# Optimization experiments

Hardware: AMD Instinct MI355X
Metric: run time of the kernel (lower is better)

The kernel has to match this reference:

```python
import jax, jax.numpy as jnp
import numpy as np

N_HEAD = 16
CHUNK = 128  # block size for the causal linear-attention scan


def _phi(x):
    return jax.nn.elu(x) + 1.0


def setup_inputs() -> dict:
    key = jax.random.key(0)
    k1, k2, k3 = jax.random.split(key, 3)
    B, T, E = 4, 2048, 1024
    x = jax.random.normal(k1, (B, T, E), dtype=jnp.float32)
    w_attn = jax.random.normal(k2, (3 * E, E), dtype=jnp.float32) * 0.02
    w_proj = jax.random.normal(k3, (E, E), dtype=jnp.float32) * 0.02
    return {"x": x, "w_attn": w_attn, "w_proj": w_proj}


def _causal_linear_attn(qp, kp, v):
    # qp, kp, v: [B, H, T, D]; phi already applied to qp, kp
    B, H, T, D = qp.shape
    NC = T // CHUNK

    def to_chunks(a):  # -> [NC, B, H, CHUNK, D]
        return a.reshape(B, H, NC, CHUNK, D).transpose(2, 0, 1, 3, 4)

    qc, kc, vc = to_chunks(qp), to_chunks(kp), to_chunks(v)
    mask = jnp.tril(jnp.ones((CHUNK, CHUNK), dtype=bool))

    def step(carry, blk):
        S, z = carry  # S: [B,H,D,D] = sum_{prev} k v^T ; z: [B,H,D] = sum_{prev} k
        q_c, k_c, v_c = blk  # [B,H,CHUNK,D]
        scores = jnp.einsum('bhcd,bhkd->bhck', q_c, k_c)
        scores = jnp.where(mask, scores, 0.0)
        num = (jnp.einsum('bhck,bhke->bhce', scores, v_c)
               + jnp.einsum('bhcd,bhde->bhce', q_c, S))
        den = scores.sum(-1) + jnp.einsum('bhcd,bhd->bhc', q_c, z)
        S = S + jnp.einsum('bhkd,bhke->bhde', k_c, v_c)
        z = z + k_c.sum(axis=2)
        return (S, z), (num, den)

    S0 = jnp.zeros((B, H, D, D), dtype=qp.dtype)
    z0 = jnp.zeros((B, H, D), dtype=qp.dtype)
    _, (num, den) = jax.lax.scan(step, (S0, z0), (qc, kc, vc))
    y = num / (den[..., None] + 1e-6)  # [NC,B,H,CHUNK,D]
    y = y.transpose(1, 2, 0, 3, 4).reshape(B, H, T, D)
    return y


def reference(x, w_attn, w_proj):
    B, T, E = x.shape
    H = N_HEAD
    D = E // H
    qkv = x @ w_attn.T  # [B,T,3E]
    q, k, v = jnp.split(qkv, 3, axis=2)

    def heads(a):  # [B,T,E] -> [B,H,T,D]
        return a.reshape(B, T, H, D).transpose(0, 2, 1, 3)

    y = _causal_linear_attn(_phi(heads(q)), _phi(heads(k)), heads(v))
    y = y.transpose(0, 2, 1, 3).reshape(B, T, E)
    return y @ w_proj.T
```

## Files before the change

### kernel.cpp

```cpp
#include <hip/hip_runtime.h>
#include <math.h>

#define B_ 4
#define T_ 2048
#define E_ 1024
#define H_ 16
#define D_ 64
#define CHUNK_ 128
#define NC_ 16
#define BH_ (B_ * H_)
#define M_ (B_ * T_)

typedef __attribute__((ext_vector_type(8))) short bf16x8;
typedef __attribute__((ext_vector_type(4))) float f32x4;

__device__ __forceinline__ ushort rnbf(float f) {
  unsigned u = __float_as_uint(f);
  unsigned r = (u + 0x7FFFu + ((u >> 16) & 1u)) >> 16;
  return (ushort)r;
}

__device__ __forceinline__ float bf2f(short s) {
  return __uint_as_float(((unsigned)(ushort)s) << 16);
}

__device__ __forceinline__ void gload_lds16(const void* g, void* l) {
  __builtin_amdgcn_global_load_lds(
      (const __attribute__((address_space(1))) unsigned int*)g,
      (__attribute__((address_space(3))) unsigned int*)l, 16, 0, 0);
}

#define VMW(N) do { asm volatile("s_waitcnt vmcnt(" #N ")" ::: "memory"); \
                    __builtin_amdgcn_sched_barrier(0); } while (0)
#define BARR() do { __builtin_amdgcn_s_barrier(); \
                    __builtin_amdgcn_sched_barrier(0); } while (0)
#define LGK0() do { asm volatile("s_waitcnt lgkmcnt(0)" ::: "memory"); \
                    __builtin_amdgcn_sched_barrier(0); } while (0)

#define N4X_ (M_ * E_ / 4)
#define N4A_ (3 * E_ * E_ / 4)
#define N4P_ (E_ * E_ / 4)
__global__ __launch_bounds__(256) void k_cvt3(
    const float* __restrict__ x, const float* __restrict__ wa,
    const float* __restrict__ wp, ushort* __restrict__ xb,
    ushort* __restrict__ wab, ushort* __restrict__ wpb) {
  int i = blockIdx.x * 256 + threadIdx.x;
  const float* src;
  ushort* dst;
  int off;
  if (i < N4X_) { src = x; dst = xb; off = i; }
  else if (i < N4X_ + N4A_) { src = wa; dst = wab; off = i - N4X_; }
  else { src = wp; dst = wpb; off = i - (N4X_ + N4A_); }
  float4 v = ((const float4*)src)[off];
  ushort4 o;
  o.x = rnbf(v.x); o.y = rnbf(v.y); o.z = rnbf(v.z); o.w = rnbf(v.w);
  ((ushort4*)dst)[off] = o;
}

#define ABASE(sl_) ((sl_) * 4096)
#define BBASE(sl_) (8192 + (sl_) * 8192)

#define STG(sl_, tt_) { \
  gload_lds16(Asrc + (tt_) * 32, &lds[ABASE(sl_) + tid * 8]); \
  gload_lds16(Bsrc0 + (tt_) * 32, &lds[BBASE(sl_) + tid * 8]); \
  gload_lds16(Bsrc1 + (tt_) * 32, &lds[BBASE(sl_) + tid * 8 + 4096]); }

#define LDFRAGS(sl_) \
  const ushort* pa = &lds[ABASE(sl_) + aOff]; \
  a0 = *(const bf16x8*)pa;          a1 = *(const bf16x8*)(pa + 512); \
  a2 = *(const bf16x8*)(pa + 1024); a3 = *(const bf16x8*)(pa + 1536); \
  const ushort* pb = &lds[BBASE(sl_) + bOff]; \
  b0 = *(const bf16x8*)pb;          b1 = *(const bf16x8*)(pb + 512); \
  b2 = *(const bf16x8*)(pb + 1024); b3 = *(const bf16x8*)(pb + 1536);

#define MM(i, j, A_, B_) \
  acc[i][j] = __builtin_amdgcn_mfma_f32_16x16x32_bf16(A_, B_, acc[i][j], 0, 0, 0)
#define MFMA16() do { __builtin_amdgcn_s_setprio(1); \
  MM(0,0,a0,b0); MM(0,1,a0,b1); MM(0,2,a0,b2); MM(0,3,a0,b3); \
  MM(1,0,a1,b0); MM(1,1,a1,b1); MM(1,2,a1,b2); MM(1,3,a1,b3); \
  MM(2,0,a2,b0); MM(2,1,a2,b1); MM(2,2,a2,b2); MM(2,3,a2,b3); \
  MM(3,0,a3,b0); MM(3,1,a3,b1); MM(3,2,a3,b2); MM(3,3,a3,b3); \
  __builtin_amdgcn_s_setprio(0); } while (0)

__device__ __forceinline__ void pipe_gemm(const ushort* __restrict__ Ag,
                                          const ushort* __restrict__ Bg,
                                          ushort* lds, f32x4 acc[4][4]) {
  const int tid = threadIdx.x;
  const int l = tid & 63, wv = tid >> 6;
  const int wm = wv >> 2, wn = wv & 3;
  const int c16 = l & 15, g4 = l >> 4;
  const int gch = (tid & 3) ^ ((tid >> 3) & 3);
  const ushort* Asrc = Ag + (size_t)(tid >> 2) * 1024 + gch * 8;
  const ushort* Bsrc0 = Bg + (size_t)(tid >> 2) * 1024 + gch * 8;
  const ushort* Bsrc1 = Bsrc0 + (size_t)128 * 1024;
  const int xq = (c16 >> 1) & 3;
  const int aOff = (wm * 64 + c16) * 32 + ((g4 ^ xq) << 3);
  const int bOff = (wn * 64 + c16) * 32 + ((g4 ^ xq) << 3);

  STG(0, 0);
  STG(1, 1);
#pragma unroll 2
  for (int t = 0; t < 30; ++t) {
    const int sl = t & 1;
    VMW(3); BARR();
    bf16x8 a0, a1, a2, a3, b0, b1, b2, b3;
    LDFRAGS(sl);
    MFMA16();
    BARR();
    STG(sl, t + 2);
  }
  {
    VMW(3); BARR();
    bf16x8 a0, a1, a2, a3, b0, b1, b2, b3;
    LDFRAGS(0);
    MFMA16();
  }
  {
    VMW(0); BARR();
    bf16x8 a0, a1, a2, a3, b0, b1, b2, b3;
    LDFRAGS(1);
    MFMA16();
  }
}

__global__ __launch_bounds__(512, 4) void k_qkv2(
    const ushort* __restrict__ xb, const ushort* __restrict__ wab,
    ushort* __restrict__ qg, ushort* __restrict__ kg,
    ushort* __restrict__ ktg, ushort* __restrict__ vtg,
    float* __restrict__ zp) {
  extern __shared__ ushort lds[];
  const int b = blockIdx.x;
  const int xcd = b & 7, idx = b >> 3;
  const int bm = xcd * 8 + (idx & 7);
  const int bn = idx >> 3;
  const int tid = threadIdx.x;
  const int wv = tid >> 6, l = tid & 63;
  const int wm = wv >> 2, wn = wv & 3;
  const int c16 = l & 15, g4 = l >> 4;

  f32x4 acc[4][4] = {};
  pipe_gemm(xb + (size_t)bm * 128 * 1024, wab + (size_t)bn * 256 * 1024, lds, acc);

  BARR();
  const int colbase = bn * 256 + wn * 64;
  const int which = colbase >> 10;
  const int h = (colbase & 1023) >> 6;
  const int rowbase = bm * 128 + wm * 64;
  const int bidx = rowbase >> 11;
  const int tbase = rowbase & 2047;
  const size_t bh = (size_t)(bidx * 16 + h);
  ushort* wlds2 = &lds[8192 + wv * 2048];
  ushort* tg = (which == 1) ? ktg : vtg;
  float zpart[4] = {0.f, 0.f, 0.f, 0.f};
#pragma unroll
  for (int p = 0; p < 2; ++p) {
#pragma unroll
    for (int mh = 0; mh < 2; ++mh) {
      const int mf = p * 2 + mh;
#pragma unroll
      for (int nf = 0; nf < 4; ++nf) {
        float o[4];
#pragma unroll
        for (int j = 0; j < 4; ++j) {
          float u = acc[mf][nf][j];
          o[j] = (which < 2) ? ((u > 0.f) ? u + 1.f : expf(u)) : u;
        }
        const int d = nf * 16 + c16;
        if (which == 1) zpart[nf] += o[0] + o[1] + o[2] + o[3];
        if (which <= 1) {
          ushort* dst = (which == 0) ? qg : kg;
          const size_t rb = (bh * 2048 + tbase + mf * 16 + g4 * 4) * 64 + d;
#pragma unroll
          for (int j = 0; j < 4; ++j) dst[rb + (size_t)j * 64] = rnbf(o[j]);
        }
        if (which >= 1) {
          const int tb2 = (mh * 4 + g4) ^ (d & 7);
          ushort4 pk;
          pk.x = rnbf(o[0]); pk.y = rnbf(o[1]); pk.z = rnbf(o[2]); pk.w = rnbf(o[3]);
          *(ushort4*)&wlds2[d * 32 + tb2 * 4] = pk;
        }
      }
    }
    if (which >= 1) {
      LGK0();
#pragma unroll
      for (int rt = 0; rt < 4; ++rt) {
        const int d = rt * 16 + (l >> 2);
        const int t0 = (l & 3) * 8;
        const int ba = ((l & 3) * 2) ^ (d & 7);
        const int bb = ((l & 3) * 2 + 1) ^ (d & 7);
        ushort4 ua = *(const ushort4*)&wlds2[d * 32 + ba * 4];
        ushort4 ub = *(const ushort4*)&wlds2[d * 32 + bb * 4];
        __align__(16) ushort tmp[8] = {ua.x, ua.y, ua.z, ua.w,
                                       ub.x, ub.y, ub.z, ub.w};
        *(bf16x8*)&tg[(bh * 64 + d) * 2048 + tbase + p * 32 + t0] =
            *(const bf16x8*)tmp;
      }
      LGK0();
    }
  }
  if (which == 1) {
    const int cc = tbase >> 7;
#pragma unroll
    for (int nf = 0; nf < 4; ++nf) {
      float zz = zpart[nf];
      zz += __shfl_xor(zz, 16);
      zz += __shfl_xor(zz, 32);
      if (l < 16) zp[((bh * NC_ + cc) * 2 + wm) * 64 + nf * 16 + l] = zz;
    }
  }
}

__global__ __launch_bounds__(512, 4) void k_proj2(
    const ushort* __restrict__ yb, const ushort* __restrict__ wpb,
    float* __restrict__ out) {
  extern __shared__ ushort lds[];
  const int b = blockIdx.x;
  const int xcd = b & 7, idx = b >> 3;
  const int bm = xcd * 8 + (idx & 7);
  const int bn = idx >> 3;
  const int tid = threadIdx.x;
  const int wv = tid >> 6, l = tid & 63;
  const int wm = wv >> 2, wn = wv & 3;
  const int c16 = l & 15, g4 = l >> 4;

  f32x4 acc[4][4] = {};
  pipe_gemm(yb + (size_t)bm * 128 * 1024, wpb + (size_t)bn * 256 * 1024, lds, acc);

  const int rowbase = bm * 128 + wm * 64 + g4 * 4;
  const int colbase = bn * 256 + wn * 64 + c16;
#pragma unroll
  for (int mf = 0; mf < 4; ++mf)
#pragma unroll
    for (int nf = 0; nf < 4; ++nf) {
      const size_t base = (size_t)(rowbase + mf * 16) * 1024 + colbase + nf * 16;
#pragma unroll
      for (int j = 0; j < 4; ++j)
        out[base + (size_t)j * 1024] = acc[mf][nf][j];
    }
}

__global__ __launch_bounds__(256) void k_stats(const ushort* __restrict__ ktg,
                                               const ushort* __restrict__ vtg,
                                               float* __restrict__ Sc) {
  __shared__ __align__(16) ushort kT_s[64 * 128], vT_s[64 * 128];
  const int blk = blockIdx.x;
  const int bh = blk >> 4, c = blk & 15;
  const int tid = threadIdx.x;
  const int w = tid >> 6, l = tid & 63;
  const ushort* ktb = ktg + (size_t)bh * D_ * T_ + c * CHUNK_;
  const ushort* vtb = vtg + (size_t)bh * D_ * T_ + c * CHUNK_;
#pragma unroll
  for (int s2 = 0; s2 < 4; ++s2) {
    const int seg = w * 4 + s2;
    const int row = seg * 4 + (l >> 4);
    const int sb = ((l & 15) ^ (row & 7)) * 8;
    gload_lds16(ktb + (size_t)row * T_ + sb, &kT_s[seg * 512]);
    gload_lds16(vtb + (size_t)row * T_ + sb, &vT_s[seg * 512]);
  }
  __syncthreads();
  const int wr = w >> 1, wc = w & 1;
  f32x4 acc[2][2] = {};
#pragma unroll
  for (int kt = 0; kt < 4; ++kt) {
    const int g = kt * 32 + (l >> 4) * 8;
    bf16x8 av[2], bk[2];
#pragma unroll
    for (int rt = 0; rt < 2; ++rt) {
      const int e = wr * 32 + rt * 16 + (l & 15);
      av[rt] = *(const bf16x8*)&vT_s[e * 128 + (g ^ ((e & 7) << 3))];
    }
#pragma unroll
    for (int ct = 0; ct < 2; ++ct) {
      const int d = wc * 32 + ct * 16 + (l & 15);
      bk[ct] = *(const bf16x8*)&kT_s[d * 128 + (g ^ ((d & 7) << 3))];
    }
#pragma unroll
    for (int rt = 0; rt < 2; ++rt)
#pragma unroll
      for (int ct = 0; ct < 2; ++ct)
        acc[rt][ct] = __builtin_amdgcn_mfma_f32_16x16x32_bf16(av[rt], bk[ct],
                                                              acc[rt][ct], 0, 0, 0);
  }
  float* So = Sc + (size_t)blk * 4096;
#pragma unroll
  for (int rt = 0; rt < 2; ++rt)
#pragma unroll
    for (int ct = 0; ct < 2; ++ct)
#pragma unroll
      for (int jj = 0; jj < 4; ++jj)
        So[(wr * 32 + rt * 16 + (l >> 4) * 4 + jj) * 64 + wc * 32 + ct * 16 + (l & 15)] =
            acc[rt][ct][jj];
}

__global__ __launch_bounds__(256) void k_prefix2(const float* __restrict__ Sc,
                                                 ushort* __restrict__ STb,
                                                 const float* __restrict__ zp,
                                                 float* __restrict__ zout) {
  const int b = blockIdx.x;
  const int tid = threadIdx.x;
  if (b < 256) {
    const int bh = b >> 2, qt = b & 3;
    const float4* Sb = (const float4*)(Sc + (size_t)bh * NC_ * 4096) + qt * 256 + tid;
    ushort4* Ob = (ushort4*)(STb + (size_t)bh * NC_ * 4096) + qt * 256 + tid;
    float4 v[16];
#pragma unroll
    for (int c = 0; c < NC_; ++c) v[c] = Sb[c * 1024];
    float4 acc = make_float4(0.f, 0.f, 0.f, 0.f);
#pragma unroll
    for (int c = 0; c < NC_; ++c) {
      ushort4 o;
      o.x = rnbf(acc.x); o.y = rnbf(acc.y); o.z = rnbf(acc.z); o.w = rnbf(acc.w);
      Ob[c * 1024] = o;
      acc.x += v[c].x; acc.y += v[c].y; acc.z += v[c].z; acc.w += v[c].w;
    }
  } else {
    const int bh = b - 256;
    if (tid < 16) {
      const float4* zpb = (const float4*)(zp + (size_t)bh * NC_ * 128);
      float4* zob = (float4*)(zout + (size_t)bh * NC_ * 64);
      float4 t0[16], t1[16];
#pragma unroll
      for (int c = 0; c < NC_; ++c) {
        t0[c] = zpb[c * 32 + tid];
        t1[c] = zpb[c * 32 + 16 + tid];
      }
      float4 za = make_float4(0.f, 0.f, 0.f, 0.f);
#pragma unroll
      for (int c = 0; c < NC_; ++c) {
        zob[c * 16 + tid] = za;
        za.x += t0[c].x + t1[c].x; za.y += t0[c].y + t1[c].y;
        za.z += t0[c].z + t1[c].z; za.w += t0[c].w + t1[c].w;
      }
    }
  }
}

__global__ __launch_bounds__(512, 4) void k_out(
    const ushort* __restrict__ qg, const ushort* __restrict__ kg,
    const ushort* __restrict__ vtg, const ushort* __restrict__ STb,
    const float* __restrict__ zg, ushort* __restrict__ yb) {
  __shared__ __align__(16) ushort k_s[128 * 64];
  __shared__ __align__(16) ushort vT_s[64 * 128];
  __shared__ __align__(16) ushort ST_s[64 * 64];
  __shared__ __align__(16) ushort P_s[128 * 128];
  __shared__ float z_s[64];
  __shared__ float dinter_s[128];
  const int blk = blockIdx.x;
  const int bh = blk >> 4, c = blk & 15;
  const int tid = threadIdx.x;
  const int w = tid >> 6, l = tid & 63;

  const ushort* kbase = kg + ((size_t)bh * T_ + c * CHUNK_) * D_;
  const ushort* vbase = vtg + (size_t)bh * D_ * T_ + c * CHUNK_;
  const ushort* sbase = STb + ((size_t)bh * NC_ + c) * 4096;
  {
    int seg = w, row = seg * 8 + (l >> 3);
    gload_lds16(kbase + (size_t)row * 64 + ((l & 7) ^ (row & 7)) * 8, &k_s[seg * 512]);
    seg = w + 8; row = seg * 8 + (l >> 3);
    gload_lds16(kbase + (size_t)row * 64 + ((l & 7) ^ (row & 7)) * 8, &k_s[seg * 512]);
  }
  {
    int seg = w, row = seg * 4 + (l >> 4);
    gload_lds16(vbase + (size_t)row * T_ + ((l & 15) ^ (row & 7)) * 8, &vT_s[seg * 512]);
    seg = w + 8; row = seg * 4 + (l >> 4);
    gload_lds16(vbase + (size_t)row * T_ + ((l & 15) ^ (row & 7)) * 8, &vT_s[seg * 512]);
  }
  {
    const int seg = w, row = seg * 8 + (l >> 3);
    gload_lds16(sbase + (size_t)row * 64 + ((l & 7) ^ (row & 7)) * 8, &ST_s[seg * 512]);
  }
  if (tid < 64) z_s[tid] = zg[((size_t)bh * NC_ + c) * 64 + tid];
  const int arow = w * 16 + (l & 15);
  const ushort* qrow = qg + ((size_t)bh * T_ + c * CHUNK_ + arow) * D_ + (l >> 4) * 8;
  bf16x8 qf0 = *(const bf16x8*)(qrow);
  bf16x8 qf1 = *(const bf16x8*)(qrow + 32);
  __syncthreads();

  f32x4 sc[8] = {};
#pragma unroll
  for (int jt = 0; jt < 8; ++jt) {
    const int j = jt * 16 + (l & 15);
    const int sw = (j & 7) << 3, g = (l >> 4) * 8;
    bf16x8 b0 = *(const bf16x8*)&k_s[j * 64 + (g ^ sw)];
    bf16x8 b1 = *(const bf16x8*)&k_s[j * 64 + ((g + 32) ^ sw)];
    sc[jt] = __builtin_amdgcn_mfma_f32_16x16x32_bf16(qf0, b0, sc[jt], 0, 0, 0);
    sc[jt] = __builtin_amdgcn_mfma_f32_16x16x32_bf16(qf1, b1, sc[jt], 0, 0, 0);
  }
  const int crow0 = w * 16 + (l >> 4) * 4;
  float rsum[4] = {0.f, 0.f, 0.f, 0.f};
#pragma unroll
  for (int jt = 0; jt < 8; ++jt) {
    const int j = jt * 16 + (l & 15);
#pragma unroll
    for (int jj = 0; jj < 4; ++jj) {
      const int i = crow0 + jj;
      float s = (j <= i) ? sc[jt][jj] : 0.f;
      rsum[jj] += s;
      P_s[i * 128 + (j ^ ((i & 7) << 3))] = rnbf(s);
    }
  }
  float di = 0.f;
#pragma unroll
  for (int jj = 0; jj < 8; ++jj) {
    di = fmaf(bf2f(qf0[jj]), z_s[(l >> 4) * 8 + jj], di);
    di = fmaf(bf2f(qf1[jj]), z_s[32 + (l >> 4) * 8 + jj], di);
  }
  di += __shfl_xor(di, 16);
  di += __shfl_xor(di, 32);
  if (l < 16) dinter_s[w * 16 + l] = di;
#pragma unroll
  for (int jj = 0; jj < 4; ++jj) {
    float r = rsum[jj];
    r += __shfl_xor(r, 1); r += __shfl_xor(r, 2);
    r += __shfl_xor(r, 4); r += __shfl_xor(r, 8);
    rsum[jj] = r;
  }
  __syncthreads();

  f32x4 acc2[4] = {};
#pragma unroll
  for (int et = 0; et < 4; ++et) {
    const int e = et * 16 + (l & 15);
    const int sw = (e & 7) << 3, g = (l >> 4) * 8;
    bf16x8 s0 = *(const bf16x8*)&ST_s[e * 64 + (g ^ sw)];
    bf16x8 s1 = *(const bf16x8*)&ST_s[e * 64 + ((g + 32) ^ sw)];
    acc2[et] = __builtin_amdgcn_mfma_f32_16x16x32_bf16(qf0, s0, acc2[et], 0, 0, 0);
    acc2[et] = __builtin_amdgcn_mfma_f32_16x16x32_bf16(qf1, s1, acc2[et], 0, 0, 0);
  }
  const int prow = w * 16 + (l & 15);
  const int psw = (prow & 7) << 3;
#pragma unroll
  for (int jkt = 0; jkt < 4; ++jkt) {
    bf16x8 pa = *(const bf16x8*)&P_s[prow * 128 + ((jkt * 32 + (l >> 4) * 8) ^ psw)];
#pragma unroll
    for (int et = 0; et < 4; ++et) {
      const int e = et * 16 + (l & 15);
      bf16x8 bv = *(const bf16x8*)&vT_s[e * 128 +
                                        ((jkt * 32 + (l >> 4) * 8) ^ ((e & 7) << 3))];
      acc2[et] = __builtin_amdgcn_mfma_f32_16x16x32_bf16(pa, bv, acc2[et], 0, 0, 0);
    }
  }
  float inv[4];
#pragma unroll
  for (int jj = 0; jj < 4; ++jj)
    inv[jj] = 1.0f / (rsum[jj] + dinter_s[crow0 + jj] + 1e-6f);
  const int b = bh >> 4, h = bh & 15;
#pragma unroll
  for (int et = 0; et < 4; ++et) {
    const int d = et * 16 + (l & 15);
#pragma unroll
    for (int jj = 0; jj < 4; ++jj) {
      const int t = c * CHUNK_ + crow0 + jj;
      yb[((size_t)(b * T_ + t) * H_ + h) * D_ + d] = rnbf(acc2[et][jj] * inv[jj]);
    }
  }
}

extern "C" void kernel_launch(void* const* d_in, const int* in_sizes, int n_in,
                              void* d_out, int out_size, void* d_ws, size_t ws_size,
                              hipStream_t stream) {
  const float* x = (const float*)d_in[0];
  const float* w_attn = (const float*)d_in[1];
  const float* w_proj = (const float*)d_in[2];
  float* out = (float*)d_out;

  ushort* xb = (ushort*)d_ws;
  ushort* wab = xb + (size_t)M_ * E_;
  ushort* wpb = wab + (size_t)3 * E_ * E_;
  ushort* qb = wpb + (size_t)E_ * E_;
  ushort* kbm = qb + (size_t)M_ * E_;
  ushort* kT = kbm + (size_t)M_ * E_;
  ushort* vT = kT + (size_t)M_ * E_;
  ushort* yb = vT + (size_t)M_ * E_;
  ushort* STb = yb + (size_t)M_ * E_;
  float* Schunk = (float*)(STb + (size_t)BH_ * NC_ * 4096);
  float* zpart = Schunk + (size_t)BH_ * NC_ * 4096;
  float* zout = zpart + (size_t)BH_ * NC_ * 2 * 64;

  k_cvt3<<<12288, 256, 0, stream>>>(x, w_attn, w_proj, xb, wab, wpb);

  hipFuncSetAttribute((const void*)k_qkv2,
                      hipFuncAttributeMaxDynamicSharedMemorySize, 49152);
  hipFuncSetAttribute((const void*)k_proj2,
                      hipFuncAttributeMaxDynamicSharedMemorySize, 49152);

  k_qkv2<<<768, 512, 49152, stream>>>(xb, wab, qb, kbm, kT, vT, zpart);
  k_stats<<<1024, 256, 0, stream>>>(kT, vT, Schunk);
  k_prefix2<<<320, 256, 0, stream>>>(Schunk, STb, zpart, zout);
  k_out<<<1024, 512, 0, stream>>>(qb, kbm, vT, STb, zout, yb);
  k_proj2<<<256, 512, 49152, stream>>>(yb, wpb, out);
}
```

Before: 132.4 us.

## Enlarge QKV GEMM tile to 256x256 with deeper K-step and 128KB LDS

Replaces the 128x256-tile QKV projection GEMM with a 256x256 tile that consumes 64-wide K steps per double-buffered stage and uses 128KB of dynamic LDS. Each wave now computes 128x64 outputs, which raises arithmetic intensity and halves global/LDS operand traffic per flop. It also adds setprio around MFMA bursts. Because each wave now covers a whole 128-row chunk, the per-chunk z partial shrinks from two halves to one, and the prefix kernel is simplified to match. The costs are fewer blocks (384, about 1.5 per CU), lower occupancy from launch_bounds(512,2) plus large LDS, and higher register pressure from 32 accumulators.

```diff
diff --git a/kernel.cpp b/kernel.cpp
--- a/kernel.cpp
+++ b/kernel.cpp
@@ -39,7 +39,6 @@
 
 #define N4X_ (M_ * E_ / 4)
 #define N4A_ (3 * E_ * E_ / 4)
-#define N4P_ (E_ * E_ / 4)
 __global__ __launch_bounds__(256) void k_cvt3(
     const float* __restrict__ x, const float* __restrict__ wa,
     const float* __restrict__ wp, ushort* __restrict__ xb,
@@ -57,6 +56,153 @@
   ((ushort4*)dst)[off] = o;
 }
 
+#define STG3(buf_, tt_) { \
+  gload_lds16(Asrc3  + (size_t)(tt_) * 64,          &lds[(buf_) * 32768 + tid * 8]); \
+  gload_lds16(Asrc3  + (size_t)(tt_) * 64 + 131072, &lds[(buf_) * 32768 + 4096 + tid * 8]); \
+  gload_lds16(Asrc3b + (size_t)(tt_) * 64,          &lds[(buf_) * 32768 + 8192 + tid * 8]); \
+  gload_lds16(Asrc3b + (size_t)(tt_) * 64 + 131072, &lds[(buf_) * 32768 + 12288 + tid * 8]); \
+  gload_lds16(Bsrc3  + (size_t)(tt_) * 64,          &lds[(buf_) * 32768 + 16384 + tid * 8]); \
+  gload_lds16(Bsrc3  + (size_t)(tt_) * 64 + 131072, &lds[(buf_) * 32768 + 20480 + tid * 8]); \
+  gload_lds16(Bsrc3b + (size_t)(tt_) * 64,          &lds[(buf_) * 32768 + 24576 + tid * 8]); \
+  gload_lds16(Bsrc3b + (size_t)(tt_) * 64 + 131072, &lds[(buf_) * 32768 + 28672 + tid * 8]); }
+
+#define MM3(i, j, A_, B_) \
+  acc[i][j] = __builtin_amdgcn_mfma_f32_16x16x32_bf16(A_, B_, acc[i][j], 0, 0, 0)
+
+#define CMP_KH(buf_, kh_) do { \
+  const ushort* ap_ = &lds[(buf_) * 32768 + (kh_) * 8192 + aB3]; \
+  const ushort* bp_ = &lds[(buf_) * 32768 + 16384 + (kh_) * 8192 + bB3]; \
+  bf16x8 B0 = *(const bf16x8*)bp_;          bf16x8 B1 = *(const bf16x8*)(bp_ + 512); \
+  bf16x8 B2 = *(const bf16x8*)(bp_ + 1024); bf16x8 B3 = *(const bf16x8*)(bp_ + 1536); \
+  bf16x8 A0 = *(const bf16x8*)ap_;          bf16x8 A1 = *(const bf16x8*)(ap_ + 512); \
+  bf16x8 A2 = *(const bf16x8*)(ap_ + 1024); bf16x8 A3 = *(const bf16x8*)(ap_ + 1536); \
+  __builtin_amdgcn_s_setprio(1); \
+  MM3(0,0,A0,B0); MM3(0,1,A0,B1); MM3(0,2,A0,B2); MM3(0,3,A0,B3); \
+  MM3(1,0,A1,B0); MM3(1,1,A1,B1); MM3(1,2,A1,B2); MM3(1,3,A1,B3); \
+  MM3(2,0,A2,B0); MM3(2,1,A2,B1); MM3(2,2,A2,B2); MM3(2,3,A2,B3); \
+  MM3(3,0,A3,B0); MM3(3,1,A3,B1); MM3(3,2,A3,B2); MM3(3,3,A3,B3); \
+  __builtin_amdgcn_s_setprio(0); \
+  bf16x8 A4 = *(const bf16x8*)(ap_ + 2048); bf16x8 A5 = *(const bf16x8*)(ap_ + 2560); \
+  bf16x8 A6 = *(const bf16x8*)(ap_ + 3072); bf16x8 A7 = *(const bf16x8*)(ap_ + 3584); \
+  __builtin_amdgcn_s_setprio(1); \
+  MM3(4,0,A4,B0); MM3(4,1,A4,B1); MM3(4,2,A4,B2); MM3(4,3,A4,B3); \
+  MM3(5,0,A5,B0); MM3(5,1,A5,B1); MM3(5,2,A5,B2); MM3(5,3,A5,B3); \
+  MM3(6,0,A6,B0); MM3(6,1,A6,B1); MM3(6,2,A6,B2); MM3(6,3,A6,B3); \
+  MM3(7,0,A7,B0); MM3(7,1,A7,B1); MM3(7,2,A7,B2); MM3(7,3,A7,B3); \
+  __builtin_amdgcn_s_setprio(0); \
+} while (0)
+
+#define COMPUTE3(buf_) do { CMP_KH(buf_, 0); CMP_KH(buf_, 1); } while (0)
+
+__global__ __launch_bounds__(512, 2) void k_qkv3(
+    const ushort* __restrict__ xb, const ushort* __restrict__ wab,
+    ushort* __restrict__ qg, ushort* __restrict__ kg,
+    ushort* __restrict__ ktg, ushort* __restrict__ vtg,
+    float* __restrict__ zp) {
+  extern __shared__ ushort lds[];
+  const int b = blockIdx.x;
+  const int xcd = b & 7, idx = b >> 3;
+  const int bm = xcd * 4 + (idx & 3);
+  const int bn = idx >> 2;
+  const int tid = threadIdx.x;
+  const int wv = tid >> 6, l = tid & 63;
+  const int wm = wv >> 2, wn = wv & 3;
+  const int c16 = l & 15, g4 = l >> 4;
+
+  const ushort* Ag = xb + (size_t)bm * 256 * 1024;
+  const ushort* Bg = wab + (size_t)bn * 256 * 1024;
+  const int cswz = ((tid & 3) ^ ((tid >> 3) & 3)) * 8;
+  const ushort* Asrc3 = Ag + (size_t)(tid >> 2) * 1024 + cswz;
+  const ushort* Asrc3b = Asrc3 + 32;
+  const ushort* Bsrc3 = Bg + (size_t)(tid >> 2) * 1024 + cswz;
+  const ushort* Bsrc3b = Bsrc3 + 32;
+  const int xcol = (g4 ^ ((c16 >> 1) & 3)) * 8;
+  const int aB3 = (wm * 128 + c16) * 32 + xcol;
+  const int bB3 = (wn * 64 + c16) * 32 + xcol;
+
+  f32x4 acc[8][4] = {};
+
+  STG3(0, 0);
+  STG3(1, 1);
+#pragma unroll 2
+  for (int t = 0; t < 14; ++t) {
+    VMW(8); BARR();
+    COMPUTE3(t & 1);
+    BARR();
+    STG3(t & 1, t + 2);
+  }
+  { VMW(8); BARR(); COMPUTE3(0); }
+  { VMW(0); BARR(); COMPUTE3(1); }
+
+  const int colbase = bn * 256 + wn * 64;
+  const int which = colbase >> 10;
+  const int h = (colbase & 1023) >> 6;
+  const int rowbase = bm * 256 + wm * 128;
+  const int bidx = rowbase >> 11;
+  const int tbase = rowbase & 2047;
+  const int cc = tbase >> 7;
+  const size_t bh = (size_t)(bidx * 16 + h);
+  ushort* wlds2 = &lds[wv * 2048];
+  ushort* tg = (which == 1) ? ktg : vtg;
+  float zpart[4] = {0.f, 0.f, 0.f, 0.f};
+#pragma unroll
+  for (int p = 0; p < 4; ++p) {
+#pragma unroll
+    for (int mh = 0; mh < 2; ++mh) {
+      const int mf = p * 2 + mh;
+#pragma unroll
+      for (int nf = 0; nf < 4; ++nf) {
+        float o[4];
+#pragma unroll
+        for (int j = 0; j < 4; ++j) {
+          float u = acc[mf][nf][j];
+          o[j] = (which < 2) ? ((u > 0.f) ? u + 1.f : expf(u)) : u;
+        }
+        const int d = nf * 16 + c16;
+        if (which == 1) zpart[nf] += o[0] + o[1] + o[2] + o[3];
+        if (which <= 1) {
+          ushort* dst = (which == 0) ? qg : kg;
+          const size_t rb = (bh * 2048 + tbase + mf * 16 + g4 * 4) * 64 + d;
+#pragma unroll
+          for (int j = 0; j < 4; ++j) dst[rb + (size_t)j * 64] = rnbf(o[j]);
+        }
+        if (which >= 1) {
+          const int tb2 = (mh * 4 + g4) ^ (d & 7);
+          ushort4 pk;
+          pk.x = rnbf(o[0]); pk.y = rnbf(o[1]); pk.z = rnbf(o[2]); pk.w = rnbf(o[3]);
+          *(ushort4*)&wlds2[d * 32 + tb2 * 4] = pk;
+        }
+      }
+    }
+    if (which >= 1) {
+      LGK0();
+#pragma unroll
+      for (int rt = 0; rt < 4; ++rt) {
+        const int d = rt * 16 + (l >> 2);
+        const int t0 = (l & 3) * 8;
+        const int ba = ((l & 3) * 2) ^ (d & 7);
+        const int bb = ((l & 3) * 2 + 1) ^ (d & 7);
+        ushort4 ua = *(const ushort4*)&wlds2[d * 32 + ba * 4];
+        ushort4 ub = *(const ushort4*)&wlds2[d * 32 + bb * 4];
+        __align__(16) ushort tmp[8] = {ua.x, ua.y, ua.z, ua.w,
+                                       ub.x, ub.y, ub.z, ub.w};
+        *(bf16x8*)&tg[(bh * 64 + d) * 2048 + tbase + p * 32 + t0] =
+            *(const bf16x8*)tmp;
+      }
+      LGK0();
+    }
+  }
+  if (which == 1) {
+#pragma unroll
+    for (int nf = 0; nf < 4; ++nf) {
+      float zz = zpart[nf];
+      zz += __shfl_xor(zz, 16);
+      zz += __shfl_xor(zz, 32);
+      if (l < 16) zp[((bh * NC_ + cc)) * 64 + nf * 16 + l] = zz;
+    }
+  }
+}
+
 #define ABASE(sl_) ((sl_) * 4096)
 #define BBASE(sl_) (8192 + (sl_) * 8192)
 
@@ -123,94 +269,6 @@
   }
 }
 
-__global__ __launch_bounds__(512, 4) void k_qkv2(
-    const ushort* __restrict__ xb, const ushort* __restrict__ wab,
-    ushort* __restrict__ qg, ushort* __restrict__ kg,
-    ushort* __restrict__ ktg, ushort* __restrict__ vtg,
-    float* __restrict__ zp) {
-  extern __shared__ ushort lds[];
-  const int b = blockIdx.x;
-  const int xcd = b & 7, idx = b >> 3;
-  const int bm = xcd * 8 + (idx & 7);
-  const int bn = idx >> 3;
-  const int tid = threadIdx.x;
-  const int wv = tid >> 6, l = tid & 63;
-  const int wm = wv >> 2, wn = wv & 3;
-  const int c16 = l & 15, g4 = l >> 4;
-
-  f32x4 acc[4][4] = {};
-  pipe_gemm(xb + (size_t)bm * 128 * 1024, wab + (size_t)bn * 256 * 1024, lds, acc);
-
-  BARR();
-  const int colbase = bn * 256 + wn * 64;
-  const int which = colbase >> 10;
-  const int h = (colbase & 1023) >> 6;
-  const int rowbase = bm * 128 + wm * 64;
-  const int bidx = rowbase >> 11;
-  const int tbase = rowbase & 2047;
-  const size_t bh = (size_t)(bidx * 16 + h);
-  ushort* wlds2 = &lds[8192 + wv * 2048];
-  ushort* tg = (which == 1) ? ktg : vtg;
-  float zpart[4] = {0.f, 0.f, 0.f, 0.f};
-#pragma unroll
-  for (int p = 0; p < 2; ++p) {
-#pragma unroll
-    for (int mh = 0; mh < 2; ++mh) {
-      const int mf = p * 2 + mh;
-#pragma unroll
-      for (int nf = 0; nf < 4; ++nf) {
-        float o[4];
-#pragma unroll
-        for (int j = 0; j < 4; ++j) {
-          float u = acc[mf][nf][j];
-          o[j] = (which < 2) ? ((u > 0.f) ? u + 1.f : expf(u)) : u;
-        }
-        const int d = nf * 16 + c16;
-        if (which == 1) zpart[nf] += o[0] + o[1] + o[2] + o[3];
-        if (which <= 1) {
-          ushort* dst = (which == 0) ? qg : kg;
-          const size_t rb = (bh * 2048 + tbase + mf * 16 + g4 * 4) * 64 + d;
-#pragma unroll
-          for (int j = 0; j < 4; ++j) dst[rb + (size_t)j * 64] = rnbf(o[j]);
-        }
-        if (which >= 1) {
-          const int tb2 = (mh * 4 + g4) ^ (d & 7);
-          ushort4 pk;
-          pk.x = rnbf(o[0]); pk.y = rnbf(o[1]); pk.z = rnbf(o[2]); pk.w = rnbf(o[3]);
-          *(ushort4*)&wlds2[d * 32 + tb2 * 4] = pk;
-        }
-      }
-    }
-    if (which >= 1) {
-      LGK0();
-#pragma unroll
-      for (int rt = 0; rt < 4; ++rt) {
-        const int d = rt * 16 + (l >> 2);
-        const int t0 = (l & 3) * 8;
-        const int ba = ((l & 3) * 2) ^ (d & 7);
-        const int bb = ((l & 3) * 2 + 1) ^ (d & 7);
-        ushort4 ua = *(const ushort4*)&wlds2[d * 32 + ba * 4];
-        ushort4 ub = *(const ushort4*)&wlds2[d * 32 + bb * 4];
-        __align__(16) ushort tmp[8] = {ua.x, ua.y, ua.z, ua.w,
-                                       ub.x, ub.y, ub.z, ub.w};
-        *(bf16x8*)&tg[(bh * 64 + d) * 2048 + tbase + p * 32 + t0] =
-            *(const bf16x8*)tmp;
-      }
-      LGK0();
-    }
-  }
-  if (which == 1) {
-    const int cc = tbase >> 7;
-#pragma unroll
-    for (int nf = 0; nf < 4; ++nf) {
-      float zz = zpart[nf];
-      zz += __shfl_xor(zz, 16);
-      zz += __shfl_xor(zz, 32);
-      if (l < 16) zp[((bh * NC_ + cc) * 2 + wm) * 64 + nf * 16 + l] = zz;
-    }
-  }
-}
-
 __global__ __launch_bounds__(512, 4) void k_proj2(
     const ushort* __restrict__ yb, const ushort* __restrict__ wpb,
     float* __restrict__ out) {
@@ -317,20 +375,17 @@
   } else {
     const int bh = b - 256;
     if (tid < 16) {
-      const float4* zpb = (const float4*)(zp + (size_t)bh * NC_ * 128);
+      const float4* zpb = (const float4*)(zp + (size_t)bh * NC_ * 64);
       float4* zob = (float4*)(zout + (size_t)bh * NC_ * 64);
-      float4 t0[16], t1[16];
-#pragma unroll
-      for (int c = 0; c < NC_; ++c) {
-        t0[c] = zpb[c * 32 + tid];
-        t1[c] = zpb[c * 32 + 16 + tid];
-      }
+      float4 t0[16];
+#pragma unroll
+      for (int c = 0; c < NC_; ++c) t0[c] = zpb[c * 16 + tid];
       float4 za = make_float4(0.f, 0.f, 0.f, 0.f);
 #pragma unroll
       for (int c = 0; c < NC_; ++c) {
         zob[c * 16 + tid] = za;
-        za.x += t0[c].x + t1[c].x; za.y += t0[c].y + t1[c].y;
-        za.z += t0[c].z + t1[c].z; za.w += t0[c].w + t1[c].w;
+        za.x += t0[c].x; za.y += t0[c].y;
+        za.z += t0[c].z; za.w += t0[c].w;
       }
     }
   }
@@ -476,16 +531,16 @@
   ushort* STb = yb + (size_t)M_ * E_;
   float* Schunk = (float*)(STb + (size_t)BH_ * NC_ * 4096);
   float* zpart = Schunk + (size_t)BH_ * NC_ * 4096;
-  float* zout = zpart + (size_t)BH_ * NC_ * 2 * 64;
+  float* zout = zpart + (size_t)BH_ * NC_ * 64;
 
   k_cvt3<<<12288, 256, 0, stream>>>(x, w_attn, w_proj, xb, wab, wpb);
 
-  hipFuncSetAttribute((const void*)k_qkv2,
-                      hipFuncAttributeMaxDynamicSharedMemorySize, 49152);
+  hipFuncSetAttribute((const void*)k_qkv3,
+                      hipFuncAttributeMaxDynamicSharedMemorySize, 131072);
   hipFuncSetAttribute((const void*)k_proj2,
                       hipFuncAttributeMaxDynamicSharedMemorySize, 49152);
 
-  k_qkv2<<<768, 512, 49152, stream>>>(xb, wab, qb, kbm, kT, vT, zpart);
+  k_qkv3<<<384, 512, 131072, stream>>>(xb, wab, qb, kbm, kT, vT, zpart);
   k_stats<<<1024, 256, 0, stream>>>(kT, vT, Schunk);
   k_prefix2<<<320, 256, 0, stream>>>(Schunk, STb, zpart, zout);
   k_out<<<1024, 512, 0, stream>>>(qb, kbm, vT, STb, zout, yb);
```

Result: slower. 148.3 us (+12.0%).

## Replace QKV GEMM with 256x256-tile triple-buffered kernel and simplify z partials

Applied to the files above, without the earlier changes.

The QKV projection GEMM moves from 128x256 tiles to 256x256 tiles, with a new three-stage LDS pipeline, an XOR-swizzled LDS layout, split A/B staging interleaved with MFMA clusters, and setprio hints. Each wave now covers 128 rows, so one z partial per chunk replaces two, and the prefix kernel and workspace layout are updated to match. Larger tiles raise arithmetic intensity and cut global traffic for the weight and activation operands. In exchange there are fewer blocks (384), lower occupancy (2 blocks per CU, 96KB LDS) and more register pressure from 32 accumulators.

```diff
diff --git a/kernel.cpp b/kernel.cpp
--- a/kernel.cpp
+++ b/kernel.cpp
@@ -39,7 +39,6 @@
 
 #define N4X_ (M_ * E_ / 4)
 #define N4A_ (3 * E_ * E_ / 4)
-#define N4P_ (E_ * E_ / 4)
 __global__ __launch_bounds__(256) void k_cvt3(
     const float* __restrict__ x, const float* __restrict__ wa,
     const float* __restrict__ wp, ushort* __restrict__ xb,
@@ -57,6 +56,195 @@
   ((ushort4*)dst)[off] = o;
 }
 
+#define QBUF(b_) ((b_) * 16384)
+
+#define STG4A(buf_, tt_) { \
+  gload_lds16(Asrc4 + (size_t)(tt_) * 32,          &lds[QBUF(buf_) + tid * 8]); \
+  gload_lds16(Asrc4 + (size_t)(tt_) * 32 + 131072, &lds[QBUF(buf_) + 4096 + tid * 8]); }
+#define STG4B(buf_, tt_) { \
+  gload_lds16(Bsrc4 + (size_t)(tt_) * 32,          &lds[QBUF(buf_) + 8192 + tid * 8]); \
+  gload_lds16(Bsrc4 + (size_t)(tt_) * 32 + 131072, &lds[QBUF(buf_) + 12288 + tid * 8]); }
+
+#define MMQ(i, j, A_, B_) \
+  acc[i][j] = __builtin_amdgcn_mfma_f32_16x16x32_bf16(A_, B_, acc[i][j], 0, 0, 0)
+
+#define CL16(Aa, Ab, Ac, Ad, i0, i1, i2, i3) do { \
+  __builtin_amdgcn_s_setprio(1); \
+  MMQ(i0,0,Aa,B0); MMQ(i0,1,Aa,B1); MMQ(i0,2,Aa,B2); MMQ(i0,3,Aa,B3); \
+  MMQ(i1,0,Ab,B0); MMQ(i1,1,Ab,B1); MMQ(i1,2,Ab,B2); MMQ(i1,3,Ab,B3); \
+  MMQ(i2,0,Ac,B0); MMQ(i2,1,Ac,B1); MMQ(i2,2,Ac,B2); MMQ(i2,3,Ac,B3); \
+  MMQ(i3,0,Ad,B0); MMQ(i3,1,Ad,B1); MMQ(i3,2,Ad,B2); MMQ(i3,3,Ad,B3); \
+  __builtin_amdgcn_s_setprio(0); } while (0)
+
+__global__ __launch_bounds__(512, 2) void k_qkv4(
+    const ushort* __restrict__ xb, const ushort* __restrict__ wab,
+    ushort* __restrict__ qg, ushort* __restrict__ kg,
+    ushort* __restrict__ ktg, ushort* __restrict__ vtg,
+    float* __restrict__ zp) {
+  extern __shared__ ushort lds[];
+  const int b = blockIdx.x;
+  const int xcd = b & 7, idx = b >> 3;
+  const int bm = xcd * 4 + (idx & 3);
+  const int bn = idx >> 2;
+  const int tid = threadIdx.x;
+  const int wv = tid >> 6, l = tid & 63;
+  const int wm = wv >> 2, wn = wv & 3;
+  const int c16 = l & 15, g4 = l >> 4;
+
+  const ushort* Ag = xb + (size_t)bm * 256 * 1024;
+  const ushort* Bg = wab + (size_t)bn * 256 * 1024;
+  const int gch = (tid & 3) ^ ((tid >> 3) & 3);
+  const ushort* Asrc4 = Ag + (size_t)(tid >> 2) * 1024 + gch * 8;
+  const ushort* Bsrc4 = Bg + (size_t)(tid >> 2) * 1024 + gch * 8;
+  const int xcol = (g4 ^ ((c16 >> 1) & 3)) << 3;
+  const int aB4 = (wm * 128 + c16) * 32 + xcol;
+  const int bB4 = (wn * 64 + c16) * 32 + xcol;
+
+  f32x4 acc[8][4] = {};
+
+  STG4A(0, 0); STG4B(0, 0);
+  STG4A(1, 1); STG4B(1, 1);
+#pragma unroll 3
+  for (int t = 0; t < 30; ++t) {
+    const int bf = t % 3;
+    const int bn2 = (t + 2) % 3;
+    VMW(4); BARR();
+    const ushort* ap = &lds[QBUF(bf) + aB4];
+    const ushort* bp = &lds[QBUF(bf) + 8192 + bB4];
+    bf16x8 B0 = *(const bf16x8*)bp;
+    bf16x8 B1 = *(const bf16x8*)(bp + 512);
+    bf16x8 B2 = *(const bf16x8*)(bp + 1024);
+    bf16x8 B3 = *(const bf16x8*)(bp + 1536);
+    bf16x8 A0 = *(const bf16x8*)ap;
+    bf16x8 A1 = *(const bf16x8*)(ap + 512);
+    bf16x8 A2 = *(const bf16x8*)(ap + 1024);
+    bf16x8 A3 = *(const bf16x8*)(ap + 1536);
+    STG4A(bn2, t + 2);
+    BARR(); LGK0();
+    CL16(A0, A1, A2, A3, 0, 1, 2, 3);
+    BARR();
+    bf16x8 A4 = *(const bf16x8*)(ap + 2048);
+    bf16x8 A5 = *(const bf16x8*)(ap + 2560);
+    bf16x8 A6 = *(const bf16x8*)(ap + 3072);
+    bf16x8 A7 = *(const bf16x8*)(ap + 3584);
+    STG4B(bn2, t + 2);
+    BARR(); LGK0();
+    CL16(A4, A5, A6, A7, 4, 5, 6, 7);
+  }
+  {
+    VMW(4); BARR();
+    const ushort* ap = &lds[QBUF(0) + aB4];
+    const ushort* bp = &lds[QBUF(0) + 8192 + bB4];
+    bf16x8 B0 = *(const bf16x8*)bp;
+    bf16x8 B1 = *(const bf16x8*)(bp + 512);
+    bf16x8 B2 = *(const bf16x8*)(bp + 1024);
+    bf16x8 B3 = *(const bf16x8*)(bp + 1536);
+    bf16x8 A0 = *(const bf16x8*)ap;
+    bf16x8 A1 = *(const bf16x8*)(ap + 512);
+    bf16x8 A2 = *(const bf16x8*)(ap + 1024);
+    bf16x8 A3 = *(const bf16x8*)(ap + 1536);
+    BARR(); LGK0();
+    CL16(A0, A1, A2, A3, 0, 1, 2, 3);
+    BARR();
+    bf16x8 A4 = *(const bf16x8*)(ap + 2048);
+    bf16x8 A5 = *(const bf16x8*)(ap + 2560);
+    bf16x8 A6 = *(const bf16x8*)(ap + 3072);
+    bf16x8 A7 = *(const bf16x8*)(ap + 3584);
+    BARR(); LGK0();
+    CL16(A4, A5, A6, A7, 4, 5, 6, 7);
+  }
+  {
+    VMW(0); BARR();
+    const ushort* ap = &lds[QBUF(1) + aB4];
+    const ushort* bp = &lds[QBUF(1) + 8192 + bB4];
+    bf16x8 B0 = *(const bf16x8*)bp;
+    bf16x8 B1 = *(const bf16x8*)(bp + 512);
+    bf16x8 B2 = *(const bf16x8*)(bp + 1024);
+    bf16x8 B3 = *(const bf16x8*)(bp + 1536);
+    bf16x8 A0 = *(const bf16x8*)ap;
+    bf16x8 A1 = *(const bf16x8*)(ap + 512);
+    bf16x8 A2 = *(const bf16x8*)(ap + 1024);
+    bf16x8 A3 = *(const bf16x8*)(ap + 1536);
+    LGK0();
+    CL16(A0, A1, A2, A3, 0, 1, 2, 3);
+    bf16x8 A4 = *(const bf16x8*)(ap + 2048);
+    bf16x8 A5 = *(const bf16x8*)(ap + 2560);
+    bf16x8 A6 = *(const bf16x8*)(ap + 3072);
+    bf16x8 A7 = *(const bf16x8*)(ap + 3584);
+    LGK0();
+    CL16(A4, A5, A6, A7, 4, 5, 6, 7);
+  }
+
+  BARR();
+  const int colbase = bn * 256 + wn * 64;
+  const int which = colbase >> 10;
+  const int h = (colbase & 1023) >> 6;
+  const int rowbase = bm * 256 + wm * 128;
+  const int bidx = rowbase >> 11;
+  const int tbase = rowbase & 2047;
+  const int cc = tbase >> 7;
+  const size_t bh = (size_t)(bidx * 16 + h);
+  ushort* wlds2 = &lds[wv * 2048];
+  ushort* tg = (which == 1) ? ktg : vtg;
+  float zpart[4] = {0.f, 0.f, 0.f, 0.f};
+#pragma unroll
+  for (int p = 0; p < 4; ++p) {
+#pragma unroll
+    for (int mh = 0; mh < 2; ++mh) {
+      const int mf = p * 2 + mh;
+#pragma unroll
+      for (int nf = 0; nf < 4; ++nf) {
+        float o[4];
+#pragma unroll
+        for (int j = 0; j < 4; ++j) {
+          float u = acc[mf][nf][j];
+          o[j] = (which < 2) ? ((u > 0.f) ? u + 1.f : expf(u)) : u;
+        }
+        const int d = nf * 16 + c16;
+        if (which == 1) zpart[nf] += o[0] + o[1] + o[2] + o[3];
+        if (which <= 1) {
+          ushort* dst = (which == 0) ? qg : kg;
+          const size_t rb = (bh * 2048 + tbase + mf * 16 + g4 * 4) * 64 + d;
+#pragma unroll
+          for (int j = 0; j < 4; ++j) dst[rb + (size_t)j * 64] = rnbf(o[j]);
+        }
+        if (which >= 1) {
+          const int tb2 = (mh * 4 + g4) ^ (d & 7);
+          ushort4 pk;
+          pk.x = rnbf(o[0]); pk.y = rnbf(o[1]); pk.z = rnbf(o[2]); pk.w = rnbf(o[3]);
+          *(ushort4*)&wlds2[d * 32 + tb2 * 4] = pk;
+        }
+      }
+    }
+    if (which >= 1) {
+      LGK0();
+#pragma unroll
+      for (int rt = 0; rt < 4; ++rt) {
+        const int d = rt * 16 + (l >> 2);
+        const int t0 = (l & 3) * 8;
+        const int ba = ((l & 3) * 2) ^ (d & 7);
+        const int bb = ((l & 3) * 2 + 1) ^ (d & 7);
+        ushort4 ua = *(const ushort4*)&wlds2[d * 32 + ba * 4];
+        ushort4 ub = *(const ushort4*)&wlds2[d * 32 + bb * 4];
+        __align__(16) ushort tmp[8] = {ua.x, ua.y, ua.z, ua.w,
+                                       ub.x, ub.y, ub.z, ub.w};
+        *(bf16x8*)&tg[(bh * 64 + d) * 2048 + tbase + p * 32 + t0] =
+            *(const bf16x8*)tmp;
+      }
+      LGK0();
+    }
+  }
+  if (which == 1) {
+#pragma unroll
+    for (int nf = 0; nf < 4; ++nf) {
+      float zz = zpart[nf];
+      zz += __shfl_xor(zz, 16);
+      zz += __shfl_xor(zz, 32);
+      if (l < 16) zp[((bh * NC_ + cc)) * 64 + nf * 16 + l] = zz;
+    }
+  }
+}
+
 #define ABASE(sl_) ((sl_) * 4096)
 #define BBASE(sl_) (8192 + (sl_) * 8192)
 
@@ -123,94 +311,6 @@
   }
 }
 
-__global__ __launch_bounds__(512, 4) void k_qkv2(
-    const ushort* __restrict__ xb, const ushort* __restrict__ wab,
-    ushort* __restrict__ qg, ushort* __restrict__ kg,
-    ushort* __restrict__ ktg, ushort* __restrict__ vtg,
-    float* __restrict__ zp) {
-  extern __shared__ ushort lds[];
-  const int b = blockIdx.x;
-  const int xcd = b & 7, idx = b >> 3;
-  const int bm = xcd * 8 + (idx & 7);
-  const int bn = idx >> 3;
-  const int tid = threadIdx.x;
-  const int wv = tid >> 6, l = tid & 63;
-  const int wm = wv >> 2, wn = wv & 3;
-  const int c16 = l & 15, g4 = l >> 4;
-
-  f32x4 acc[4][4] = {};
-  pipe_gemm(xb + (size_t)bm * 128 * 1024, wab + (size_t)bn * 256 * 1024, lds, acc);
-
-  BARR();
-  const int colbase = bn * 256 + wn * 64;
-  const int which = colbase >> 10;
-  const int h = (colbase & 1023) >> 6;
-  const int rowbase = bm * 128 + wm * 64;
-  const int bidx = rowbase >> 11;
-  const int tbase = rowbase & 2047;
-  const size_t bh = (size_t)(bidx * 16 + h);
-  ushort* wlds2 = &lds[8192 + wv * 2048];
-  ushort* tg = (which == 1) ? ktg : vtg;
-  float zpart[4] = {0.f, 0.f, 0.f, 0.f};
-#pragma unroll
-  for (int p = 0; p < 2; ++p) {
-#pragma unroll
-    for (int mh = 0; mh < 2; ++mh) {
-      const int mf = p * 2 + mh;
-#pragma unroll
-      for (int nf = 0; nf < 4; ++nf) {
-        float o[4];
-#pragma unroll
-        for (int j = 0; j < 4; ++j) {
-          float u = acc[mf][nf][j];
-          o[j] = (which < 2) ? ((u > 0.f) ? u + 1.f : expf(u)) : u;
-        }
-        const int d = nf * 16 + c16;
-        if (which == 1) zpart[nf] += o[0] + o[1] + o[2] + o[3];
-        if (which <= 1) {
-          ushort* dst = (which == 0) ? qg : kg;
-          const size_t rb = (bh * 2048 + tbase + mf * 16 + g4 * 4) * 64 + d;
-#pragma unroll
-          for (int j = 0; j < 4; ++j) dst[rb + (size_t)j * 64] = rnbf(o[j]);
-        }
-        if (which >= 1) {
-          const int tb2 = (mh * 4 + g4) ^ (d & 7);
-          ushort4 pk;
-          pk.x = rnbf(o[0]); pk.y = rnbf(o[1]); pk.z = rnbf(o[2]); pk.w = rnbf(o[3]);
-          *(ushort4*)&wlds2[d * 32 + tb2 * 4] = pk;
-        }
-      }
-    }
-    if (which >= 1) {
-      LGK0();
-#pragma unroll
-      for (int rt = 0; rt < 4; ++rt) {
-        const int d = rt * 16 + (l >> 2);
-        const int t0 = (l & 3) * 8;
-        const int ba = ((l & 3) * 2) ^ (d & 7);
-        const int bb = ((l & 3) * 2 + 1) ^ (d & 7);
-        ushort4 ua = *(const ushort4*)&wlds2[d * 32 + ba * 4];
-        ushort4 ub = *(const ushort4*)&wlds2[d * 32 + bb * 4];
-        __align__(16) ushort tmp[8] = {ua.x, ua.y, ua.z, ua.w,
-                                       ub.x, ub.y, ub.z, ub.w};
-        *(bf16x8*)&tg[(bh * 64 + d) * 2048 + tbase + p * 32 + t0] =
-            *(const bf16x8*)tmp;
-      }
-      LGK0();
-    }
-  }
-  if (which == 1) {
-    const int cc = tbase >> 7;
-#pragma unroll
-    for (int nf = 0; nf < 4; ++nf) {
-      float zz = zpart[nf];
-      zz += __shfl_xor(zz, 16);
-      zz += __shfl_xor(zz, 32);
-      if (l < 16) zp[((bh * NC_ + cc) * 2 + wm) * 64 + nf * 16 + l] = zz;
-    }
-  }
-}
-
 __global__ __launch_bounds__(512, 4) void k_proj2(
     const ushort* __restrict__ yb, const ushort* __restrict__ wpb,
     float* __restrict__ out) {
@@ -317,20 +417,17 @@
   } else {
     const int bh = b - 256;
     if (tid < 16) {
-      const float4* zpb = (const float4*)(zp + (size_t)bh * NC_ * 128);
+      const float4* zpb = (const float4*)(zp + (size_t)bh * NC_ * 64);
       float4* zob = (float4*)(zout + (size_t)bh * NC_ * 64);
-      float4 t0[16], t1[16];
-#pragma unroll
-      for (int c = 0; c < NC_; ++c) {
-        t0[c] = zpb[c * 32 + tid];
-        t1[c] = zpb[c * 32 + 16 + tid];
-      }
+      float4 t0[16];
+#pragma unroll
+      for (int c = 0; c < NC_; ++c) t0[c] = zpb[c * 16 + tid];
       float4 za = make_float4(0.f, 0.f, 0.f, 0.f);
 #pragma unroll
       for (int c = 0; c < NC_; ++c) {
         zob[c * 16 + tid] = za;
-        za.x += t0[c].x + t1[c].x; za.y += t0[c].y + t1[c].y;
-        za.z += t0[c].z + t1[c].z; za.w += t0[c].w + t1[c].w;
+        za.x += t0[c].x; za.y += t0[c].y;
+        za.z += t0[c].z; za.w += t0[c].w;
       }
     }
   }
@@ -476,16 +573,16 @@
   ushort* STb = yb + (size_t)M_ * E_;
   float* Schunk = (float*)(STb + (size_t)BH_ * NC_ * 4096);
   float* zpart = Schunk + (size_t)BH_ * NC_ * 4096;
-  float* zout = zpart + (size_t)BH_ * NC_ * 2 * 64;
+  float* zout = zpart + (size_t)BH_ * NC_ * 64;
 
   k_cvt3<<<12288, 256, 0, stream>>>(x, w_attn, w_proj, xb, wab, wpb);
 
-  hipFuncSetAttribute((const void*)k_qkv2,
-                      hipFuncAttributeMaxDynamicSharedMemorySize, 49152);
+  hipFuncSetAttribute((const void*)k_qkv4,
+                      hipFuncAttributeMaxDynamicSharedMemorySize, 98304);
   hipFuncSetAttribute((const void*)k_proj2,
                       hipFuncAttributeMaxDynamicSharedMemorySize, 49152);
 
-  k_qkv2<<<768, 512, 49152, stream>>>(xb, wab, qb, kbm, kT, vT, zpart);
+  k_qkv4<<<384, 512, 98304, stream>>>(xb, wab, qb, kbm, kT, vT, zpart);
   k_stats<<<1024, 256, 0, stream>>>(kT, vT, Schunk);
   k_prefix2<<<320, 256, 0, stream>>>(Schunk, STb, zpart, zout);
   k_out<<<1024, 512, 0, stream>>>(qb, kbm, vT, STb, zout, yb);
```

Result: slower. 140.3 us (+5.9%).
